# Optimization experiments

Hardware: AMD Instinct MI355X
Metric: run time of the kernel (lower is better)

The kernel has to match this reference:

```python
import jax, jax.numpy as jnp
import numpy as np

B, D_IN, D_PROJ, N_CLS = 4096, 4096, 1024, 32
N_CHILD = (32, 64)


def setup_inputs() -> dict:
    key = jax.random.key(0)
    ks = jax.random.split(key, 12)
    std = 2e-05
    inp = {
        "x": jax.random.normal(ks[0], (B, D_IN), dtype=jnp.float32),
        "y": jax.random.randint(ks[1], (B,), 0, N_CLS, dtype=jnp.int32),
        # parent projection: Linear(D_IN, D_PROJ)
        "Wp": jax.random.normal(ks[2], (D_IN, D_PROJ), dtype=jnp.float32) * std,
        "bp": jnp.zeros((D_PROJ,), jnp.float32),
        # subclass projection: Linear(D_IN, D_PROJ)
        "Ws": jax.random.normal(ks[3], (D_IN, D_PROJ), dtype=jnp.float32) * std,
        "bs": jnp.zeros((D_PROJ,), jnp.float32),
        # parent classifier: Linear(D_PROJ, N_CLS)
        "Wc": jax.random.normal(ks[4], (D_PROJ, N_CLS), dtype=jnp.float32) * std,
        "bc": jnp.zeros((N_CLS,), jnp.float32),
        # child expert banks: level i has N_CLS experts of Linear(D_PROJ, N_CHILD[i])
        "cw0": jax.random.normal(ks[5], (N_CLS, N_CHILD[0], D_PROJ), dtype=jnp.float32) * std,
        "cb0": jnp.zeros((N_CLS, N_CHILD[0]), jnp.float32),
        "cw1": jax.random.normal(ks[6], (N_CLS, N_CHILD[1], D_PROJ), dtype=jnp.float32) * std,
        "cb1": jnp.zeros((N_CLS, N_CHILD[1]), jnp.float32),
    }
    return inp


def reference(x, y, Wp, bp, Ws, bs, Wc, bc, cw0, cb0, cw1, cb1):
    # dropout p = 0.0 -> identity
    parent_proj_embed = x @ Wp + bp                 # [B, D_PROJ]
    parent_logits = parent_proj_embed @ Wc + bc     # [B, N_CLS]
    child_proj_embed = x @ Ws + bs                  # [B, D_PROJ]
    # per-sample expert routing: gather the expert for label y[b], then batched matvec
    child_logits0 = jnp.einsum("bd,bnd->bn", child_proj_embed, cw0[y]) + cb0[y]  # [B, 32]
    child_logits1 = jnp.einsum("bd,bnd->bn", child_proj_embed, cw1[y]) + cb1[y]  # [B, 64]
    return (parent_logits, child_logits0, child_logits1, parent_proj_embed, child_proj_embed)
```

## Files before the change

kernel.cpp:

```cpp
#include <hip/hip_runtime.h>
#include <hip/hip_bf16.h>
#include <stdint.h>


typedef __attribute__((ext_vector_type(4))) float  floatx4;
typedef __attribute__((ext_vector_type(8))) short  shortx8;
typedef __attribute__((ext_vector_type(4))) short  shortx4;
typedef __attribute__((ext_vector_type(8))) __bf16 bf16x8;

static __device__ __forceinline__ ushort f32_to_bf16_rne(float f) {
  uint32_t u = __builtin_bit_cast(uint32_t, f);
  u += 0x7FFFu + ((u >> 16) & 1u);
  return (ushort)(u >> 16);
}

static __device__ __forceinline__ void async_copy16(const void* g, void* lds) {
  __builtin_amdgcn_global_load_lds(
      (__attribute__((address_space(1))) void*)(uintptr_t)g,
      (__attribute__((address_space(3))) void*)(uintptr_t)lds,
      16, 0, 0);
}

__global__ __launch_bounds__(256) void k_prep(
    const float* __restrict__ x,   const int* __restrict__ y,
    const float* __restrict__ Wp,  const float* __restrict__ Ws,
    const float* __restrict__ Wc,
    const float* __restrict__ cw0, const float* __restrict__ cw1,
    ushort* __restrict__ xb,  ushort* __restrict__ Bt1,
    ushort* __restrict__ cwb, ushort* __restrict__ Wcb,
    int* __restrict__ perm, int* __restrict__ offs)
{
  __shared__ __align__(16) ushort tile[64 * 72];
  __shared__ int hist[32], hbase[32], hcur[32];
  const int b = blockIdx.x;
  const int t = threadIdx.x;

  if (b == 0) {
    if (t < 32) { hist[t] = 0; hcur[t] = 0; }
    __syncthreads();
    int yv[16];
    #pragma unroll
    for (int i = 0; i < 16; ++i) { yv[i] = y[t * 16 + i]; atomicAdd(&hist[yv[i]], 1); }
    __syncthreads();
    if (t == 0) {
      int s = 0;
      for (int c = 0; c < 32; ++c) { hbase[c] = s; offs[c] = s; s += hist[c]; }
      offs[32] = s;
    }
    __syncthreads();
    #pragma unroll
    for (int i = 0; i < 16; ++i) {
      const int c = yv[i];
      const int p = atomicAdd(&hcur[c], 1);
      perm[hbase[c] + p] = t * 16 + i;
    }
  } else if (b <= 4224) {
    const int row = b - 1;
    const int k = t * 4;
    float v0 = 0.f, v1 = 0.f, v2 = 0.f, v3 = 0.f;
    ushort* dst;
    if (row < 4096) {
      const int c = row >> 7, n = row & 127;
      if (n < 32) {
        floatx4 f = *reinterpret_cast<const floatx4*>(cw0 + (size_t)(c * 32 + n) * 1024 + k);
        v0 = f[0]; v1 = f[1]; v2 = f[2]; v3 = f[3];
      } else if (n < 96) {
        floatx4 f = *reinterpret_cast<const floatx4*>(cw1 + (size_t)(c * 64 + (n - 32)) * 1024 + k);
        v0 = f[0]; v1 = f[1]; v2 = f[2]; v3 = f[3];
      }
      dst = cwb + (size_t)row * 1024 + k;
    } else {
      const int n = row - 4096;
      if (n < 32) {
        v0 = Wc[(k + 0) * 32 + n]; v1 = Wc[(k + 1) * 32 + n];
        v2 = Wc[(k + 2) * 32 + n]; v3 = Wc[(k + 3) * 32 + n];
      }
      dst = Wcb + (size_t)n * 1024 + k;
    }
    shortx4 o;
    o[0] = (short)f32_to_bf16_rne(v0); o[1] = (short)f32_to_bf16_rne(v1);
    o[2] = (short)f32_to_bf16_rne(v2); o[3] = (short)f32_to_bf16_rne(v3);
    *reinterpret_cast<shortx4*>(dst) = o;
  } else if (b <= 6272) {
    const int vt = b - 4225;
    const int z = vt >> 10, rest = vt & 1023;
    const int nt = rest >> 6, kt = rest & 63;
    const float* W = z ? Ws : Wp;
    const int r = t >> 4, c = (t & 15) * 4;
    #pragma unroll
    for (int j = 0; j < 4; ++j) {
      const int kk = r + j * 16;
      floatx4 v = *reinterpret_cast<const floatx4*>(
          W + (size_t)(kt * 64 + kk) * 1024 + nt * 64 + c);
      tile[(c + 0) * 72 + kk] = f32_to_bf16_rne(v[0]);
      tile[(c + 1) * 72 + kk] = f32_to_bf16_rne(v[1]);
      tile[(c + 2) * 72 + kk] = f32_to_bf16_rne(v[2]);
      tile[(c + 3) * 72 + kk] = f32_to_bf16_rne(v[3]);
    }
    __syncthreads();
    const int nl = t >> 3, ch = t & 7;
    #pragma unroll
    for (int j = 0; j < 2; ++j) {
      const int n = nl + j * 32;
      shortx8 v = *reinterpret_cast<const shortx8*>(tile + n * 72 + ch * 8);
      *reinterpret_cast<shortx8*>(
          Bt1 + (size_t)(z * 1024 + nt * 64 + n) * 4096 + kt * 64 + ch * 8) = v;
    }
  } else {
    const size_t i = ((size_t)(b - 6273) * 256 + t) * 8;
    floatx4 a = *reinterpret_cast<const floatx4*>(x + i);
    floatx4 c = *reinterpret_cast<const floatx4*>(x + i + 4);
    shortx8 o;
    o[0] = (short)f32_to_bf16_rne(a[0]); o[1] = (short)f32_to_bf16_rne(a[1]);
    o[2] = (short)f32_to_bf16_rne(a[2]); o[3] = (short)f32_to_bf16_rne(a[3]);
    o[4] = (short)f32_to_bf16_rne(c[0]); o[5] = (short)f32_to_bf16_rne(c[1]);
    o[6] = (short)f32_to_bf16_rne(c[2]); o[7] = (short)f32_to_bf16_rne(c[3]);
    *reinterpret_cast<shortx8*>(xb + i) = o;
  }
}

__global__ __launch_bounds__(512, 2) void k_gemm1(
    const ushort* __restrict__ xb, const ushort* __restrict__ Bt1,
    const float* __restrict__ bp, const float* __restrict__ bs,
    float* __restrict__ outP, float* __restrict__ outS,
    ushort* __restrict__ Pb, ushort* __restrict__ Sb)
{
  __shared__ __align__(16) ushort lA[3 * 256 * 64];
  __shared__ __align__(16) ushort lB[3 * 128 * 64];

  floatx4 acc[4][4];
  const floatx4 z4 = {0.f, 0.f, 0.f, 0.f};
  #pragma unroll
  for (int i = 0; i < 4; ++i)
    #pragma unroll
    for (int j = 0; j < 4; ++j) acc[i][j] = z4;

  const int t    = threadIdx.x;
  const int w    = t >> 6;
  const int lane = t & 63;
  const int wr   = w >> 1;
  const int wc   = w & 1;
  const int r16  = lane & 15;
  const int qd   = lane >> 4;

  const ushort* Abase = xb  + (size_t)(blockIdx.x * 256) * 4096;
  const ushort* Bbase = Bt1 + (size_t)(blockIdx.y * 128) * 4096;

  const int    rS   = t >> 3;
  const int    qs   = ((t & 7) ^ (rS & 7)) << 3;
  const int    dUni = (t & ~63) * 8;

  const int px0 = (0 * 4 + qd) ^ (r16 & 7);
  const int px1 = (1 * 4 + qd) ^ (r16 & 7);
  const int aRd = (wr * 64 + r16) * 64;
  const int bRd = (wc * 64 + r16) * 64;

  #define STAGE_CHUNK(slot, k0)                                                \
    do {                                                                       \
      _Pragma("unroll")                                                        \
      for (int j = 0; j < 4; ++j)                                              \
        async_copy16(Abase + (size_t)(j * 64 + rS) * 4096 + (k0) + qs,         \
                     lA + (slot) * 16384 + j * 4096 + dUni);                   \
      _Pragma("unroll")                                                        \
      for (int j = 0; j < 2; ++j)                                              \
        async_copy16(Bbase + (size_t)(j * 64 + rS) * 4096 + (k0) + qs,         \
                     lB + (slot) * 8192 + j * 4096 + dUni);                    \
    } while (0)

  STAGE_CHUNK(0, 0);
  STAGE_CHUNK(1, 64);
  asm volatile("s_waitcnt vmcnt(6)" ::: "memory");
  __builtin_amdgcn_s_barrier();
  asm volatile("" ::: "memory");

  for (int c = 0; c < 64; ++c) {
    const int slot = c % 3;
    const ushort* As = lA + slot * 16384;
    const ushort* Bs = lB + slot * 8192;

    bf16x8 af[2][4], bfv[2][4];
    #pragma unroll
    for (int mi = 0; mi < 4; ++mi) {
      af[0][mi] = *reinterpret_cast<const bf16x8*>(As + aRd + mi * 1024 + px0 * 8);
      af[1][mi] = *reinterpret_cast<const bf16x8*>(As + aRd + mi * 1024 + px1 * 8);
    }
    #pragma unroll
    for (int ni = 0; ni < 4; ++ni) {
      bfv[0][ni] = *reinterpret_cast<const bf16x8*>(Bs + bRd + ni * 1024 + px0 * 8);
      bfv[1][ni] = *reinterpret_cast<const bf16x8*>(Bs + bRd + ni * 1024 + px1 * 8);
    }

    {
      const int cs  = c + 2;
      const int ss  = cs % 3;
      const int k0s = (cs < 64 ? cs : 63) * 64;
      STAGE_CHUNK(ss, k0s);
    }

    __builtin_amdgcn_s_setprio(1);
    #pragma unroll
    for (int ks = 0; ks < 2; ++ks)
      #pragma unroll
      for (int mi = 0; mi < 4; ++mi)
        #pragma unroll
        for (int ni = 0; ni < 4; ++ni)
          acc[mi][ni] = __builtin_amdgcn_mfma_f32_16x16x32_bf16(
              af[ks][mi], bfv[ks][ni], acc[mi][ni], 0, 0, 0);
    __builtin_amdgcn_s_setprio(0);

    asm volatile("s_waitcnt vmcnt(6)" ::: "memory");
    __builtin_amdgcn_s_barrier();
    asm volatile("" ::: "memory");
  }
  #undef STAGE_CHUNK

  const int sel = (blockIdx.y >= 8);
  const float* bias = sel ? bs : bp;
  float*  outF = sel ? outS : outP;
  ushort* outB = sel ? Sb : Pb;
  const int colbase = blockIdx.y * 128 - sel * 1024;
  #pragma unroll
  for (int mi = 0; mi < 4; ++mi) {
    #pragma unroll
    for (int ni = 0; ni < 4; ++ni) {
      const int n = colbase + wc * 64 + ni * 16 + r16;
      const float bv = bias[n];
      #pragma unroll
      for (int rg = 0; rg < 4; ++rg) {
        const int m = blockIdx.x * 256 + wr * 64 + mi * 16 + qd * 4 + rg;
        const float v = acc[mi][ni][rg] + bv;
        const size_t off = (size_t)m * 1024 + n;
        outF[off] = v;
        outB[off] = f32_to_bf16_rne(v);
      }
    }
  }
}

static __device__ __forceinline__ void mfma_bk_step64(
    const ushort* lA, const ushort* lB, floatx4 acc[4][4],
    int wr, int wc, int r16, int quad)
{
  #pragma unroll
  for (int ks = 0; ks < 2; ++ks) {
    bf16x8 af[4], bfv[4];
    const int pc = (((ks * 4) + quad) ^ (r16 & 7)) * 8;
    #pragma unroll
    for (int mi = 0; mi < 4; ++mi)
      af[mi] = *reinterpret_cast<const bf16x8*>(lA + (wr * 64 + mi * 16 + r16) * 64 + pc);
    #pragma unroll
    for (int ni = 0; ni < 4; ++ni)
      bfv[ni] = *reinterpret_cast<const bf16x8*>(lB + (wc * 64 + ni * 16 + r16) * 64 + pc);
    #pragma unroll
    for (int mi = 0; mi < 4; ++mi)
      #pragma unroll
      for (int ni = 0; ni < 4; ++ni)
        acc[mi][ni] = __builtin_amdgcn_mfma_f32_16x16x32_bf16(
            af[mi], bfv[ni], acc[mi][ni], 0, 0, 0);
  }
}

__global__ __launch_bounds__(256) void k_head(
    const ushort* __restrict__ Sb, const ushort* __restrict__ Pb,
    const ushort* __restrict__ cwb, const ushort* __restrict__ Wcb,
    const int* __restrict__ perm, const int* __restrict__ off,
    const float* __restrict__ cb0, const float* __restrict__ cb1,
    const float* __restrict__ bc,
    float* __restrict__ out0, float* __restrict__ out1,
    float* __restrict__ outParent)
{
  __shared__ __align__(16) ushort lA[128 * 64];
  __shared__ __align__(16) ushort lB[128 * 64];
  floatx4 acc[4][4];
  const floatx4 z4 = {0.f, 0.f, 0.f, 0.f};
  #pragma unroll
  for (int i = 0; i < 4; ++i)
    #pragma unroll
    for (int j = 0; j < 4; ++j) acc[i][j] = z4;

  const int t = threadIdx.x, w = t >> 6, lane = t & 63;
  const int wr = w >> 1, wc = w & 1, r16 = lane & 15, quad = lane >> 4;
  const int sr = lane >> 3, sc = lane & 7;

  if (blockIdx.y == 32) {
    const ushort* Abase = Pb + (size_t)(blockIdx.x * 128) * 1024;
    for (int k0 = 0; k0 < 1024; k0 += 64) {
      #pragma unroll
      for (int c2 = 0; c2 < 4; ++c2) {
        const int r  = 32 * w + 8 * c2 + sr;
        const int gc = sc ^ sr;
        async_copy16(Abase + (size_t)r * 1024 + k0 + gc * 8, lA + (32 * w + 8 * c2) * 64);
        async_copy16(Wcb   + (size_t)r * 1024 + k0 + gc * 8, lB + (32 * w + 8 * c2) * 64);
      }
      __syncthreads();
      mfma_bk_step64(lA, lB, acc, wr, wc, r16, quad);
      __syncthreads();
    }
    if (wc == 0) {
      #pragma unroll
      for (int mi = 0; mi < 4; ++mi)
        #pragma unroll
        for (int ni = 0; ni < 2; ++ni) {
          const int n = ni * 16 + r16;
          const float bv = bc[n];
          #pragma unroll
          for (int rg = 0; rg < 4; ++rg) {
            const int m = blockIdx.x * 128 + wr * 64 + mi * 16 + quad * 4 + rg;
            outParent[(size_t)m * 32 + n] = acc[mi][ni][rg] + bv;
          }
        }
    }
    return;
  }

  const int c    = blockIdx.y;
  const int off0 = off[c];
  const int cnt  = off[c + 1] - off0;
  const int m0   = blockIdx.x * 128;
  if (m0 >= cnt) return;

  int rowSamp[4];
  #pragma unroll
  for (int c2 = 0; c2 < 4; ++c2) {
    const int r = 32 * w + 8 * c2 + sr;
    rowSamp[c2] = perm[off0 + min(m0 + r, cnt - 1)];
  }
  const ushort* Bbase = cwb + (size_t)c * 128 * 1024;

  for (int k0 = 0; k0 < 1024; k0 += 64) {
    #pragma unroll
    for (int c2 = 0; c2 < 4; ++c2) {
      const int r  = 32 * w + 8 * c2 + sr;
      const int gc = sc ^ sr;
      async_copy16(Sb + (size_t)rowSamp[c2] * 1024 + k0 + gc * 8, lA + (32 * w + 8 * c2) * 64);
      async_copy16(Bbase + (size_t)r * 1024 + k0 + gc * 8,        lB + (32 * w + 8 * c2) * 64);
    }
    __syncthreads();
    mfma_bk_step64(lA, lB, acc, wr, wc, r16, quad);
    __syncthreads();
  }

  #pragma unroll
  for (int mi = 0; mi < 4; ++mi) {
    #pragma unroll
    for (int rg = 0; rg < 4; ++rg) {
      const int gm = m0 + wr * 64 + mi * 16 + quad * 4 + rg;
      if (gm >= cnt) continue;
      const int sample = perm[off0 + gm];
      #pragma unroll
      for (int ni = 0; ni < 4; ++ni) {
        const int n = wc * 64 + ni * 16 + r16;
        if (n < 32)
          out0[(size_t)sample * 32 + n] = acc[mi][ni][rg] + cb0[c * 32 + n];
        else if (n < 96)
          out1[(size_t)sample * 64 + (n - 32)] = acc[mi][ni][rg] + cb1[c * 64 + (n - 32)];
      }
    }
  }
}


extern "C" void kernel_launch(void* const* d_in, const int* in_sizes, int n_in,
                              void* d_out, int out_size, void* d_ws, size_t ws_size,
                              hipStream_t stream) {
  const float* x   = (const float*)d_in[0];
  const int*   y   = (const int*)  d_in[1];
  const float* Wp  = (const float*)d_in[2];
  const float* bp  = (const float*)d_in[3];
  const float* Ws  = (const float*)d_in[4];
  const float* bs  = (const float*)d_in[5];
  const float* Wc  = (const float*)d_in[6];
  const float* bc  = (const float*)d_in[7];
  const float* cw0 = (const float*)d_in[8];
  const float* cb0 = (const float*)d_in[9];
  const float* cw1 = (const float*)d_in[10];
  const float* cb1 = (const float*)d_in[11];

  float* out = (float*)d_out;
  float* parent_logits = out;
  float* child0        = out + 131072;
  float* child1        = out + 262144;
  float* P             = out + 524288;
  float* S             = out + 4718592;

  char* ws = (char*)d_ws;
  ushort* xb   = (ushort*)(ws);
  ushort* Bt1  = (ushort*)(ws + 33554432);
  ushort* Pb   = (ushort*)(ws + 50331648);
  ushort* Sb   = (ushort*)(ws + 58720256);
  ushort* cwb  = (ushort*)(ws + 67108864);
  ushort* Wcb  = (ushort*)(ws + 75497472);
  int*    perm = (int*)   (ws + 75759616);
  int*    offs = (int*)   (ws + 75776000);

  k_prep <<<14465, 256, 0, stream>>>(x, y, Wp, Ws, Wc, cw0, cw1,
                                     xb, Bt1, cwb, Wcb, perm, offs);
  k_gemm1<<<dim3(16, 16), 512, 0, stream>>>(xb, Bt1, bp, bs, P, S, Pb, Sb);
  k_head <<<dim3(32, 33), 256, 0, stream>>>(Sb, Pb, cwb, Wcb, perm, offs,
                                            cb0, cb1, bc,
                                            child0, child1, parent_logits);
}
```

Before: 294.8 us.

## Triple-buffer k_head LDS loads with async prefetch and swap grid axes

```diff
diff --git a/kernel.cpp b/kernel.cpp
--- a/kernel.cpp
+++ b/kernel.cpp
@@ -237,27 +237,35 @@
   }
 }
 
-static __device__ __forceinline__ void mfma_bk_step64(
-    const ushort* lA, const ushort* lB, floatx4 acc[4][4],
+static __device__ __forceinline__ void load_frags64(
+    const ushort* lA, const ushort* lB, bf16x8 af[2][4], bf16x8 bfv[2][4],
     int wr, int wc, int r16, int quad)
 {
   #pragma unroll
   for (int ks = 0; ks < 2; ++ks) {
-    bf16x8 af[4], bfv[4];
     const int pc = (((ks * 4) + quad) ^ (r16 & 7)) * 8;
     #pragma unroll
     for (int mi = 0; mi < 4; ++mi)
-      af[mi] = *reinterpret_cast<const bf16x8*>(lA + (wr * 64 + mi * 16 + r16) * 64 + pc);
+      af[ks][mi] = *reinterpret_cast<const bf16x8*>(lA + (wr * 64 + mi * 16 + r16) * 64 + pc);
     #pragma unroll
     for (int ni = 0; ni < 4; ++ni)
-      bfv[ni] = *reinterpret_cast<const bf16x8*>(lB + (wc * 64 + ni * 16 + r16) * 64 + pc);
+      bfv[ks][ni] = *reinterpret_cast<const bf16x8*>(lB + (wc * 64 + ni * 16 + r16) * 64 + pc);
+  }
+}
+
+static __device__ __forceinline__ void mfma_frags64(
+    bf16x8 af[2][4], bf16x8 bfv[2][4], floatx4 acc[4][4])
+{
+  __builtin_amdgcn_s_setprio(1);
+  #pragma unroll
+  for (int ks = 0; ks < 2; ++ks)
     #pragma unroll
     for (int mi = 0; mi < 4; ++mi)
       #pragma unroll
       for (int ni = 0; ni < 4; ++ni)
         acc[mi][ni] = __builtin_amdgcn_mfma_f32_16x16x32_bf16(
-            af[mi], bfv[ni], acc[mi][ni], 0, 0, 0);
-  }
+            af[ks][mi], bfv[ks][ni], acc[mi][ni], 0, 0, 0);
+  __builtin_amdgcn_s_setprio(0);
 }
 
 __global__ __launch_bounds__(256) void k_head(
@@ -269,8 +277,8 @@
     float* __restrict__ out0, float* __restrict__ out1,
     float* __restrict__ outParent)
 {
-  __shared__ __align__(16) ushort lA[128 * 64];
-  __shared__ __align__(16) ushort lB[128 * 64];
+  __shared__ __align__(16) ushort lA[3 * 128 * 64];
+  __shared__ __align__(16) ushort lB[3 * 128 * 64];
   floatx4 acc[4][4];
   const floatx4 z4 = {0.f, 0.f, 0.f, 0.f};
   #pragma unroll
@@ -281,21 +289,47 @@
   const int t = threadIdx.x, w = t >> 6, lane = t & 63;
   const int wr = w >> 1, wc = w & 1, r16 = lane & 15, quad = lane >> 4;
   const int sr = lane >> 3, sc = lane & 7;
-
-  if (blockIdx.y == 32) {
-    const ushort* Abase = Pb + (size_t)(blockIdx.x * 128) * 1024;
-    for (int k0 = 0; k0 < 1024; k0 += 64) {
-      #pragma unroll
-      for (int c2 = 0; c2 < 4; ++c2) {
-        const int r  = 32 * w + 8 * c2 + sr;
-        const int gc = sc ^ sr;
-        async_copy16(Abase + (size_t)r * 1024 + k0 + gc * 8, lA + (32 * w + 8 * c2) * 64);
-        async_copy16(Wcb   + (size_t)r * 1024 + k0 + gc * 8, lB + (32 * w + 8 * c2) * 64);
+  const int gc = sc ^ sr;
+  const int dRow = 32 * w;
+
+  if (blockIdx.x == 32) {
+    const ushort* Abase = Pb + (size_t)(blockIdx.y * 128) * 1024;
+
+    #define STAGE_P(slot, k0)                                                  \
+      do {                                                                     \
+        _Pragma("unroll")                                                      \
+        for (int c2 = 0; c2 < 4; ++c2) {                                       \
+          const int r = dRow + 8 * c2 + sr;                                    \
+          async_copy16(Abase + (size_t)r * 1024 + (k0) + gc * 8,               \
+                       lA + (slot) * 8192 + (dRow + 8 * c2) * 64);             \
+          async_copy16(Wcb + (size_t)r * 1024 + (k0) + gc * 8,                 \
+                       lB + (slot) * 8192 + (dRow + 8 * c2) * 64);             \
+        }                                                                      \
+      } while (0)
+
+    STAGE_P(0, 0);
+    STAGE_P(1, 64);
+    asm volatile("s_waitcnt vmcnt(8)" ::: "memory");
+    __builtin_amdgcn_s_barrier();
+    asm volatile("" ::: "memory");
+
+    for (int c = 0; c < 16; ++c) {
+      const int slot = c % 3;
+      bf16x8 af[2][4], bfv[2][4];
+      load_frags64(lA + slot * 8192, lB + slot * 8192, af, bfv, wr, wc, r16, quad);
+      {
+        const int cs  = c + 2;
+        const int ss  = cs % 3;
+        const int k0s = (cs < 16 ? cs : 15) * 64;
+        STAGE_P(ss, k0s);
       }
-      __syncthreads();
-      mfma_bk_step64(lA, lB, acc, wr, wc, r16, quad);
-      __syncthreads();
-    }
+      mfma_frags64(af, bfv, acc);
+      asm volatile("s_waitcnt vmcnt(8)" ::: "memory");
+      __builtin_amdgcn_s_barrier();
+      asm volatile("" ::: "memory");
+    }
+    #undef STAGE_P
+
     if (wc == 0) {
       #pragma unroll
       for (int mi = 0; mi < 4; ++mi)
@@ -305,7 +339,7 @@
           const float bv = bc[n];
           #pragma unroll
           for (int rg = 0; rg < 4; ++rg) {
-            const int m = blockIdx.x * 128 + wr * 64 + mi * 16 + quad * 4 + rg;
+            const int m = blockIdx.y * 128 + wr * 64 + mi * 16 + quad * 4 + rg;
             outParent[(size_t)m * 32 + n] = acc[mi][ni][rg] + bv;
           }
         }
@@ -313,32 +347,54 @@
     return;
   }
 
-  const int c    = blockIdx.y;
-  const int off0 = off[c];
-  const int cnt  = off[c + 1] - off0;
-  const int m0   = blockIdx.x * 128;
+  const int cls  = blockIdx.x;
+  const int off0 = off[cls];
+  const int cnt  = off[cls + 1] - off0;
+  const int m0   = blockIdx.y * 128;
   if (m0 >= cnt) return;
 
   int rowSamp[4];
   #pragma unroll
   for (int c2 = 0; c2 < 4; ++c2) {
-    const int r = 32 * w + 8 * c2 + sr;
+    const int r = dRow + 8 * c2 + sr;
     rowSamp[c2] = perm[off0 + min(m0 + r, cnt - 1)];
   }
-  const ushort* Bbase = cwb + (size_t)c * 128 * 1024;
-
-  for (int k0 = 0; k0 < 1024; k0 += 64) {
-    #pragma unroll
-    for (int c2 = 0; c2 < 4; ++c2) {
-      const int r  = 32 * w + 8 * c2 + sr;
-      const int gc = sc ^ sr;
-      async_copy16(Sb + (size_t)rowSamp[c2] * 1024 + k0 + gc * 8, lA + (32 * w + 8 * c2) * 64);
-      async_copy16(Bbase + (size_t)r * 1024 + k0 + gc * 8,        lB + (32 * w + 8 * c2) * 64);
-    }
-    __syncthreads();
-    mfma_bk_step64(lA, lB, acc, wr, wc, r16, quad);
-    __syncthreads();
-  }
+  const ushort* Bbase = cwb + (size_t)cls * 128 * 1024;
+
+  #define STAGE_C(slot, k0)                                                    \
+    do {                                                                       \
+      _Pragma("unroll")                                                        \
+      for (int c2 = 0; c2 < 4; ++c2) {                                         \
+        const int r = dRow + 8 * c2 + sr;                                      \
+        async_copy16(Sb + (size_t)rowSamp[c2] * 1024 + (k0) + gc * 8,          \
+                     lA + (slot) * 8192 + (dRow + 8 * c2) * 64);               \
+        async_copy16(Bbase + (size_t)r * 1024 + (k0) + gc * 8,                 \
+                     lB + (slot) * 8192 + (dRow + 8 * c2) * 64);               \
+      }                                                                        \
+    } while (0)
+
+  STAGE_C(0, 0);
+  STAGE_C(1, 64);
+  asm volatile("s_waitcnt vmcnt(8)" ::: "memory");
+  __builtin_amdgcn_s_barrier();
+  asm volatile("" ::: "memory");
+
+  for (int c = 0; c < 16; ++c) {
+    const int slot = c % 3;
+    bf16x8 af[2][4], bfv[2][4];
+    load_frags64(lA + slot * 8192, lB + slot * 8192, af, bfv, wr, wc, r16, quad);
+    {
+      const int cs  = c + 2;
+      const int ss  = cs % 3;
+      const int k0s = (cs < 16 ? cs : 15) * 64;
+      STAGE_C(ss, k0s);
+    }
+    mfma_frags64(af, bfv, acc);
+    asm volatile("s_waitcnt vmcnt(8)" ::: "memory");
+    __builtin_amdgcn_s_barrier();
+    asm volatile("" ::: "memory");
+  }
+  #undef STAGE_C
 
   #pragma unroll
   for (int mi = 0; mi < 4; ++mi) {
@@ -351,9 +407,9 @@
       for (int ni = 0; ni < 4; ++ni) {
         const int n = wc * 64 + ni * 16 + r16;
         if (n < 32)
-          out0[(size_t)sample * 32 + n] = acc[mi][ni][rg] + cb0[c * 32 + n];
+          out0[(size_t)sample * 32 + n] = acc[mi][ni][rg] + cb0[cls * 32 + n];
         else if (n < 96)
-          out1[(size_t)sample * 64 + (n - 32)] = acc[mi][ni][rg] + cb1[c * 64 + (n - 32)];
+          out1[(size_t)sample * 64 + (n - 32)] = acc[mi][ni][rg] + cb1[cls * 64 + (n - 32)];
       }
     }
   }
@@ -396,7 +452,7 @@
   k_prep <<<14465, 256, 0, stream>>>(x, y, Wp, Ws, Wc, cw0, cw1,
                                      xb, Bt1, cwb, Wcb, perm, offs);
   k_gemm1<<<dim3(16, 16), 512, 0, stream>>>(xb, Bt1, bp, bs, P, S, Pb, Sb);
-  k_head <<<dim3(32, 33), 256, 0, stream>>>(Sb, Pb, cwb, Wcb, perm, offs,
+  k_head <<<dim3(33, 32), 256, 0, stream>>>(Sb, Pb, cwb, Wcb, perm, offs,
                                             cb0, cb1, bc,
                                             child0, child1, parent_logits);
 }
```

After: 252.5 us. 14.3% less time.
